# Kernel tuning notes

Hardware: AMD Instinct MI355X
Metric: run time of the kernel (lower is better)

## Reference

```python
import jax, jax.numpy as jnp
import numpy as np

B, N, M = 8, 4096, 4096


def setup_inputs() -> dict:
    key = jax.random.key(0)
    k1, k2 = jax.random.split(key)
    tar = jax.random.normal(k1, (B, N, 3), dtype=jnp.float32)
    src = jax.random.normal(k2, (B, M, 3), dtype=jnp.float32)
    return {"tar": tar, "src": src}


def reference(tar, src):
    # diff: [b, n, m, 3]; dist: [b, n, m] Euclidean norm
    diff = tar[:, :, None, :] - src[:, None, :, :]
    dist = jnp.sqrt(jnp.sum(diff * diff, axis=-1))
    # complete: for each target point, min over source points, mean over n -> [b]
    complete = jnp.mean(jnp.min(dist, axis=2), axis=1)
    # accuracy: for each source point, min over target points, mean over m -> [b]
    accuracy = jnp.mean(jnp.min(dist, axis=1), axis=1)
    # reduction='mean' over batch axis
    complete = jnp.mean(complete, axis=-1)
    accuracy = jnp.mean(accuracy, axis=-1)
    chamfer = 0.5 * (complete + accuracy)
    return (accuracy, complete, chamfer)
```

## Files before the change

kernel.cpp:

```cpp
#include <hip/hip_runtime.h>
#include <math.h>

#define B_ 8
#define BIGF 3.4e38f


__global__ __launch_bounds__(256) void pack_kernel(
    const float* __restrict__ tar, const float* __restrict__ src,
    float4* __restrict__ packT, float4* __restrict__ packS,
    unsigned int* __restrict__ minarr, float* __restrict__ outp,
    int N, int M)
{
    const int i = blockIdx.x * 256 + threadIdx.x;
    const int nT = B_ * N, nS = B_ * M;
    if (i < nT) {
        float x = tar[3 * i], y = tar[3 * i + 1], z = tar[3 * i + 2];
        packT[i] = make_float4(x, y, z, fmaf(x, x, fmaf(y, y, z * z)));
    } else if (i < nT + nS) {
        int j = i - nT;
        float x = src[3 * j], y = src[3 * j + 1], z = src[3 * j + 2];
        packS[j] = make_float4(x, y, z, fmaf(x, x, fmaf(y, y, z * z)));
    }
    if (i < nT + nS) minarr[i] = 0x7F800000u;
    if (i < 3) outp[i] = 0.f;
}

template <int QPT, int CHUNK>
__global__ __launch_bounds__(256) void minsq_kernel(
    const float4* __restrict__ packT, const float4* __restrict__ packS,
    unsigned int* __restrict__ minarr, int N, int M)
{
    const int z   = blockIdx.z;
    const int dir = (z >= B_) ? 1 : 0;
    const int b   = dir ? (z - B_) : z;
    const float4* __restrict__ qry = dir ? packS : packT;
    const float4* __restrict__ pts = dir ? packT : packS;
    const int K = dir ? M : N;
    const int L = dir ? N : M;
    unsigned int* __restrict__ out =
        minarr + (dir ? (size_t)B_ * N : (size_t)0) + (size_t)b * K;

    const int base = blockIdx.y * CHUNK;
    if (base >= L) return;
    const int cnt = min(CHUNK, L - base);
    const float4* __restrict__ psrc = pts + (size_t)b * L + base;

    const int t = threadIdx.x;
    const int qbase = blockIdx.x * (256 * QPT);
    float qx2[QPT], qy2[QPT], qz2[QPT], qw[QPT], mn[QPT];
#pragma unroll
    for (int k = 0; k < QPT; ++k) {
        int qi = qbase + k * 256 + t;
        if (qi < K) {
            float4 q = qry[(size_t)b * K + qi];
            qx2[k] = -2.f * q.x; qy2[k] = -2.f * q.y; qz2[k] = -2.f * q.z;
            qw[k] = q.w;
        } else {
            qx2[k] = 0.f; qy2[k] = 0.f; qz2[k] = 0.f; qw[k] = 0.f;
        }
        mn[k] = BIGF;
    }

    if (cnt == CHUNK) {
#pragma unroll 2
        for (int j = 0; j < CHUNK; j += 4) {
            float4 p0 = psrc[j];
            float4 p1 = psrc[j + 1];
            float4 p2 = psrc[j + 2];
            float4 p3 = psrc[j + 3];
#pragma unroll
            for (int k = 0; k < QPT; ++k) {
                float d0 = fmaf(qx2[k], p0.x, fmaf(qy2[k], p0.y,
                           fmaf(qz2[k], p0.z, p0.w)));
                float d1 = fmaf(qx2[k], p1.x, fmaf(qy2[k], p1.y,
                           fmaf(qz2[k], p1.z, p1.w)));
                float d2 = fmaf(qx2[k], p2.x, fmaf(qy2[k], p2.y,
                           fmaf(qz2[k], p2.z, p2.w)));
                float d3 = fmaf(qx2[k], p3.x, fmaf(qy2[k], p3.y,
                           fmaf(qz2[k], p3.z, p3.w)));
                mn[k] = fminf(mn[k], fminf(d0, d1));
                mn[k] = fminf(mn[k], fminf(d2, d3));
            }
        }
    } else {
        for (int j = 0; j < cnt; ++j) {
            float4 p0 = psrc[j];
#pragma unroll
            for (int k = 0; k < QPT; ++k) {
                float d0 = fmaf(qx2[k], p0.x, fmaf(qy2[k], p0.y,
                           fmaf(qz2[k], p0.z, p0.w)));
                mn[k] = fminf(mn[k], d0);
            }
        }
    }

#pragma unroll
    for (int k = 0; k < QPT; ++k) {
        int qi = qbase + k * 256 + t;
        if (qi < K) {
            float d2 = fmaxf(mn[k] + qw[k], 0.f);
            atomicMin(&out[qi], __float_as_uint(d2));
        }
    }
}

__global__ __launch_bounds__(256) void reduce_kernel(
    const unsigned int* __restrict__ minarr, float* __restrict__ outp,
    int N, int M)
{
    const int nt = B_ * N, ns = B_ * M;
    const int gid = blockIdx.x * 256 + threadIdx.x;
    const int stride = gridDim.x * 256;
    float s_t = 0.f, s_s = 0.f;
    for (int i = gid; i < nt; i += stride)
        s_t += sqrtf(__uint_as_float(minarr[i]));
    for (int i = gid; i < ns; i += stride)
        s_s += sqrtf(__uint_as_float(minarr[nt + i]));
#pragma unroll
    for (int off = 32; off > 0; off >>= 1) {
        s_t += __shfl_down(s_t, off);
        s_s += __shfl_down(s_s, off);
    }
    __shared__ float rt[4], rs[4];
    const int wid = threadIdx.x >> 6, lid = threadIdx.x & 63;
    if (lid == 0) { rt[wid] = s_t; rs[wid] = s_s; }
    __syncthreads();
    if (threadIdx.x == 0) {
        float ct = (rt[0] + rt[1] + rt[2] + rt[3]) / (float)nt;
        float ac = (rs[0] + rs[1] + rs[2] + rs[3]) / (float)ns;
        atomicAdd(&outp[0], ac);
        atomicAdd(&outp[1], ct);
        atomicAdd(&outp[2], 0.5f * (ac + ct));
    }
}

extern "C" void kernel_launch(void* const* d_in, const int* in_sizes, int n_in,
                              void* d_out, int out_size, void* d_ws, size_t ws_size,
                              hipStream_t stream) {
    const float* tar = (const float*)d_in[0];
    const float* src = (const float*)d_in[1];
    const int N = in_sizes[0] / (B_ * 3);
    const int M = in_sizes[1] / (B_ * 3);

    float4* packT = (float4*)d_ws;
    float4* packS = packT + (size_t)B_ * N;
    unsigned int* minarr = (unsigned int*)(packS + (size_t)B_ * M);
    float* outp = (float*)d_out;

    pack_kernel<<<dim3((B_ * (N + M) + 255) / 256), dim3(256), 0, stream>>>(
        tar, src, packT, packS, minarr, outp, N, M);

    constexpr int QPT = 8, CHUNK = 128;
    const int KL = (N > M) ? N : M;
    const int gx = (KL + 256 * QPT - 1) / (256 * QPT);
    const int gy = (KL + CHUNK - 1) / CHUNK;
    dim3 grid(gx, gy, 2 * B_);
    minsq_kernel<QPT, CHUNK><<<grid, dim3(256), 0, stream>>>(
        packT, packS, minarr, N, M);

    reduce_kernel<<<dim3(32), dim3(256), 0, stream>>>(minarr, outp, N, M);
}
```

Before: 93.20 us.

## Stage point chunk in LDS as SoA and use packed FMA with larger QPT

Each block now loads its chunk of reference points into shared memory in structure-of-arrays layout and pads the tail with a large w, which removes the separate partial-chunk path. The inner loop is written with 2-wide float vectors so the compiler can emit packed FP32 FMA instructions (v_pk_fma_f32). Queries per thread rise from 8 to 16 with launch bounds asking for 2 blocks per CU. This aims to raise arithmetic throughput and amortise point loads, at the cost of more registers, a barrier, and half as many blocks in x.

```diff
diff --git a/kernel.cpp b/kernel.cpp
--- a/kernel.cpp
+++ b/kernel.cpp
@@ -3,6 +3,9 @@
 
 #define B_ 8
 #define BIGF 3.4e38f
+
+typedef float f32x2 __attribute__((ext_vector_type(2)));
+typedef float f32x4 __attribute__((ext_vector_type(4)));
 
 
 __global__ __launch_bounds__(256) void pack_kernel(
@@ -26,7 +29,7 @@
 }
 
 template <int QPT, int CHUNK>
-__global__ __launch_bounds__(256) void minsq_kernel(
+__global__ __launch_bounds__(256, 2) void minsq_kernel(
     const float4* __restrict__ packT, const float4* __restrict__ packS,
     unsigned int* __restrict__ minarr, int N, int M)
 {
@@ -45,52 +48,69 @@
     const int cnt = min(CHUNK, L - base);
     const float4* __restrict__ psrc = pts + (size_t)b * L + base;
 
+    __shared__ __align__(16) float sx[CHUNK], sy[CHUNK], sz[CHUNK], sw[CHUNK];
     const int t = threadIdx.x;
+    for (int i = t; i < cnt; i += 256) {
+        float4 p = psrc[i];
+        sx[i] = p.x; sy[i] = p.y; sz[i] = p.z; sw[i] = p.w;
+    }
+    for (int i = cnt + t; i < CHUNK; i += 256) {
+        sx[i] = 0.f; sy[i] = 0.f; sz[i] = 0.f; sw[i] = BIGF;
+    }
+    __syncthreads();
+
     const int qbase = blockIdx.x * (256 * QPT);
-    float qx2[QPT], qy2[QPT], qz2[QPT], qw[QPT], mn[QPT];
+    f32x2 qx[QPT], qy[QPT], qz[QPT];
+    float qw[QPT], mn[QPT];
 #pragma unroll
     for (int k = 0; k < QPT; ++k) {
         int qi = qbase + k * 256 + t;
+        float ax = 0.f, ay = 0.f, az = 0.f, aw = 0.f;
         if (qi < K) {
             float4 q = qry[(size_t)b * K + qi];
-            qx2[k] = -2.f * q.x; qy2[k] = -2.f * q.y; qz2[k] = -2.f * q.z;
-            qw[k] = q.w;
-        } else {
-            qx2[k] = 0.f; qy2[k] = 0.f; qz2[k] = 0.f; qw[k] = 0.f;
+            ax = -2.f * q.x; ay = -2.f * q.y; az = -2.f * q.z; aw = q.w;
         }
+        qx[k].x = ax; qx[k].y = ax;
+        qy[k].x = ay; qy[k].y = ay;
+        qz[k].x = az; qz[k].y = az;
+        qw[k] = aw;
         mn[k] = BIGF;
     }
 
-    if (cnt == CHUNK) {
+    const f32x4* __restrict__ X4 = (const f32x4*)sx;
+    const f32x4* __restrict__ Y4 = (const f32x4*)sy;
+    const f32x4* __restrict__ Z4 = (const f32x4*)sz;
+    const f32x4* __restrict__ W4 = (const f32x4*)sw;
+
 #pragma unroll 2
-        for (int j = 0; j < CHUNK; j += 4) {
-            float4 p0 = psrc[j];
-            float4 p1 = psrc[j + 1];
-            float4 p2 = psrc[j + 2];
-            float4 p3 = psrc[j + 3];
+    for (int j4 = 0; j4 < CHUNK / 4; ++j4) {
+        f32x4 X = X4[j4], Y = Y4[j4], Z = Z4[j4], W = W4[j4];
+        f32x2 x01; x01.x = X.x; x01.y = X.y;
+        f32x2 x23; x23.x = X.z; x23.y = X.w;
+        f32x2 y01; y01.x = Y.x; y01.y = Y.y;
+        f32x2 y23; y23.x = Y.z; y23.y = Y.w;
+        f32x2 z01; z01.x = Z.x; z01.y = Z.y;
+        f32x2 z23; z23.x = Z.z; z23.y = Z.w;
+        f32x2 w01; w01.x = W.x; w01.y = W.y;
+        f32x2 w23; w23.x = W.z; w23.y = W.w;
 #pragma unroll
-            for (int k = 0; k < QPT; ++k) {
-                float d0 = fmaf(qx2[k], p0.x, fmaf(qy2[k], p0.y,
-                           fmaf(qz2[k], p0.z, p0.w)));
-                float d1 = fmaf(qx2[k], p1.x, fmaf(qy2[k], p1.y,
-                           fmaf(qz2[k], p1.z, p1.w)));
-                float d2 = fmaf(qx2[k], p2.x, fmaf(qy2[k], p2.y,
-                           fmaf(qz2[k], p2.z, p2.w)));
-                float d3 = fmaf(qx2[k], p3.x, fmaf(qy2[k], p3.y,
-                           fmaf(qz2[k], p3.z, p3.w)));
-                mn[k] = fminf(mn[k], fminf(d0, d1));
-                mn[k] = fminf(mn[k], fminf(d2, d3));
-            }
-        }
-    } else {
-        for (int j = 0; j < cnt; ++j) {
-            float4 p0 = psrc[j];
-#pragma unroll
-            for (int k = 0; k < QPT; ++k) {
-                float d0 = fmaf(qx2[k], p0.x, fmaf(qy2[k], p0.y,
-                           fmaf(qz2[k], p0.z, p0.w)));
-                mn[k] = fminf(mn[k], d0);
-            }
+        for (int k = 0; k < QPT; ++k) {
+#if __has_builtin(__builtin_elementwise_fma)
+            f32x2 dA = __builtin_elementwise_fma(qx[k], x01,
+                       __builtin_elementwise_fma(qy[k], y01,
+                       __builtin_elementwise_fma(qz[k], z01, w01)));
+            f32x2 dB = __builtin_elementwise_fma(qx[k], x23,
+                       __builtin_elementwise_fma(qy[k], y23,
+                       __builtin_elementwise_fma(qz[k], z23, w23)));
+#else
+            f32x2 dA, dB;
+            dA.x = fmaf(qx[k].x, x01.x, fmaf(qy[k].x, y01.x, fmaf(qz[k].x, z01.x, w01.x)));
+            dA.y = fmaf(qx[k].y, x01.y, fmaf(qy[k].y, y01.y, fmaf(qz[k].y, z01.y, w01.y)));
+            dB.x = fmaf(qx[k].x, x23.x, fmaf(qy[k].x, y23.x, fmaf(qz[k].x, z23.x, w23.x)));
+            dB.y = fmaf(qx[k].y, x23.y, fmaf(qy[k].y, y23.y, fmaf(qz[k].y, z23.y, w23.y)));
+#endif
+            mn[k] = fminf(fminf(dA.x, dA.y), mn[k]);
+            mn[k] = fminf(fminf(dB.x, dB.y), mn[k]);
         }
     }
 
@@ -150,7 +170,7 @@
     pack_kernel<<<dim3((B_ * (N + M) + 255) / 256), dim3(256), 0, stream>>>(
         tar, src, packT, packS, minarr, outp, N, M);
 
-    constexpr int QPT = 8, CHUNK = 128;
+    constexpr int QPT = 16, CHUNK = 128;
     const int KL = (N > M) ? N : M;
     const int gx = (KL + 256 * QPT - 1) / (256 * QPT);
     const int gy = (KL + CHUNK - 1) / CHUNK;
```

Measured after the change: 86.50 us. -7.2%, faster.

## Load source points via scalar dwordx16 loads and halve chunk size

Applied to the files above, without the earlier changes.

Replaces the per-thread float4 vector loads of uniform source points with inline-asm s_load_dwordx16 scalar loads into SGPRs, 16 points at a time. The w term is forced into a VGPR so the FMA chains can consume SGPR operands. Also sets a launch_bounds occupancy hint and halves CHUNK, which doubles the grid and the number of atomicMin writes. The scalar loads wait fully on lgkmcnt each group, which serialises memory latency with compute.

```diff
diff --git a/kernel.cpp b/kernel.cpp
--- a/kernel.cpp
+++ b/kernel.cpp
@@ -3,6 +3,8 @@
 
 #define B_ 8
 #define BIGF 3.4e38f
+
+typedef float f32x16 __attribute__((ext_vector_type(16)));
 
 
 __global__ __launch_bounds__(256) void pack_kernel(
@@ -25,8 +27,17 @@
     if (i < 3) outp[i] = 0.f;
 }
 
+#define LOAD_GROUP(A, B, C, D, PTR)                                       \
+    asm volatile("s_load_dwordx16 %0, %4, 0x0\n\t"                        \
+                 "s_load_dwordx16 %1, %4, 0x40\n\t"                       \
+                 "s_load_dwordx16 %2, %4, 0x80\n\t"                       \
+                 "s_load_dwordx16 %3, %4, 0xc0\n\t"                       \
+                 "s_waitcnt lgkmcnt(0)"                                   \
+                 : "=s"(A), "=s"(B), "=s"(C), "=s"(D)                     \
+                 : "s"(PTR))
+
 template <int QPT, int CHUNK>
-__global__ __launch_bounds__(256) void minsq_kernel(
+__global__ __launch_bounds__(256, 8) void minsq_kernel(
     const float4* __restrict__ packT, const float4* __restrict__ packS,
     unsigned int* __restrict__ minarr, int N, int M)
 {
@@ -47,48 +58,55 @@
 
     const int t = threadIdx.x;
     const int qbase = blockIdx.x * (256 * QPT);
-    float qx2[QPT], qy2[QPT], qz2[QPT], qw[QPT], mn[QPT];
+    float qx[QPT], qy[QPT], qz[QPT], qw[QPT], mn[QPT];
 #pragma unroll
     for (int k = 0; k < QPT; ++k) {
         int qi = qbase + k * 256 + t;
         if (qi < K) {
             float4 q = qry[(size_t)b * K + qi];
-            qx2[k] = -2.f * q.x; qy2[k] = -2.f * q.y; qz2[k] = -2.f * q.z;
+            qx[k] = -2.f * q.x; qy[k] = -2.f * q.y; qz[k] = -2.f * q.z;
             qw[k] = q.w;
         } else {
-            qx2[k] = 0.f; qy2[k] = 0.f; qz2[k] = 0.f; qw[k] = 0.f;
+            qx[k] = 0.f; qy[k] = 0.f; qz[k] = 0.f; qw[k] = 0.f;
         }
         mn[k] = BIGF;
     }
 
     if (cnt == CHUNK) {
-#pragma unroll 2
-        for (int j = 0; j < CHUNK; j += 4) {
-            float4 p0 = psrc[j];
-            float4 p1 = psrc[j + 1];
-            float4 p2 = psrc[j + 2];
-            float4 p3 = psrc[j + 3];
 #pragma unroll
-            for (int k = 0; k < QPT; ++k) {
-                float d0 = fmaf(qx2[k], p0.x, fmaf(qy2[k], p0.y,
-                           fmaf(qz2[k], p0.z, p0.w)));
-                float d1 = fmaf(qx2[k], p1.x, fmaf(qy2[k], p1.y,
-                           fmaf(qz2[k], p1.z, p1.w)));
-                float d2 = fmaf(qx2[k], p2.x, fmaf(qy2[k], p2.y,
-                           fmaf(qz2[k], p2.z, p2.w)));
-                float d3 = fmaf(qx2[k], p3.x, fmaf(qy2[k], p3.y,
-                           fmaf(qz2[k], p3.z, p3.w)));
-                mn[k] = fminf(mn[k], fminf(d0, d1));
-                mn[k] = fminf(mn[k], fminf(d2, d3));
+        for (int g = 0; g < CHUNK / 16; ++g) {
+            f32x16 A, Bv, C, D;
+            LOAD_GROUP(A, Bv, C, D, psrc + g * 16);
+#define PAIR(R, i0, i1)                                                   \
+            {                                                             \
+                float s0x = R[4*(i0)+0], s0y = R[4*(i0)+1],               \
+                      s0z = R[4*(i0)+2], v0w = R[4*(i0)+3];               \
+                float s1x = R[4*(i1)+0], s1y = R[4*(i1)+1],               \
+                      s1z = R[4*(i1)+2], v1w = R[4*(i1)+3];               \
+                asm("" : "+v"(v0w));   \
+                asm("" : "+v"(v1w));                                      \
+                _Pragma("unroll")                                         \
+                for (int k = 0; k < QPT; ++k) {                           \
+                    float d0 = fmaf(qx[k], s0x, fmaf(qy[k], s0y,          \
+                               fmaf(qz[k], s0z, v0w)));                   \
+                    float d1 = fmaf(qx[k], s1x, fmaf(qy[k], s1y,          \
+                               fmaf(qz[k], s1z, v1w)));                   \
+                    mn[k] = fminf(fminf(d0, d1), mn[k]);      \
+                }                                                         \
             }
+            PAIR(A, 0, 1)  PAIR(A, 2, 3)
+            PAIR(Bv, 0, 1) PAIR(Bv, 2, 3)
+            PAIR(C, 0, 1)  PAIR(C, 2, 3)
+            PAIR(D, 0, 1)  PAIR(D, 2, 3)
+#undef PAIR
         }
     } else {
         for (int j = 0; j < cnt; ++j) {
             float4 p0 = psrc[j];
 #pragma unroll
             for (int k = 0; k < QPT; ++k) {
-                float d0 = fmaf(qx2[k], p0.x, fmaf(qy2[k], p0.y,
-                           fmaf(qz2[k], p0.z, p0.w)));
+                float d0 = fmaf(qx[k], p0.x, fmaf(qy[k], p0.y,
+                           fmaf(qz[k], p0.z, p0.w)));
                 mn[k] = fminf(mn[k], d0);
             }
         }
@@ -150,7 +168,7 @@
     pack_kernel<<<dim3((B_ * (N + M) + 255) / 256), dim3(256), 0, stream>>>(
         tar, src, packT, packS, minarr, outp, N, M);
 
-    constexpr int QPT = 8, CHUNK = 128;
+    constexpr int QPT = 8, CHUNK = 64;
     const int KL = (N > M) ? N : M;
     const int gx = (KL + 256 * QPT - 1) / (256 * QPT);
     const int gy = (KL + CHUNK - 1) / CHUNK;
```

Measured after the change: 89.03 us. 4.5% less time.
